# Optimization experiments

Measured on AMD Instinct MI355X. Metric: run time of the kernel, lower is better.

Reference implementation:

```python
import jax, jax.numpy as jnp
import numpy as np

IN_FEATURES = 4096
OUT_FEATURES = 11008
GROUP_SIZE = 32
M_TOKENS = 32
Q_MID = 8  # int4 midpoint: dequant = (q - 8) * scale + zero


def setup_inputs() -> dict:
    key = jax.random.key(0)
    k1, k2, k3, k4 = jax.random.split(key, 4)
    n_groups = IN_FEATURES // GROUP_SIZE
    inputs = {
        "input": jax.random.normal(k1, (M_TOKENS, IN_FEATURES), dtype=jnp.float32),
        "weight": jax.random.randint(k2, (OUT_FEATURES, IN_FEATURES), 0, 16, dtype=jnp.int32),
        "scales_and_zeros": jax.random.normal(k3, (n_groups, OUT_FEATURES, 2), dtype=jnp.float32),
        "bias": jax.random.normal(k4, (OUT_FEATURES,), dtype=jnp.float32),
        "group_size": GROUP_SIZE,
    }
    return inputs


def reference(input, weight, scales_and_zeros, bias, group_size):
    out_features, in_features = weight.shape
    n_groups = in_features // group_size
    # scales/zeros per (group, out) -> [out, n_groups]
    scale = scales_and_zeros[..., 0].T  # [out, G]
    zero = scales_and_zeros[..., 1].T   # [out, G]
    # dequantize int4 weight: w = (q - 8) * scale + zero, per group along in_features
    q = weight.astype(jnp.float32).reshape(out_features, n_groups, group_size)
    w_fp = (q - Q_MID) * scale[:, :, None] + zero[:, :, None]  # [out, G, gs]
    w_fp = w_fp.reshape(out_features, in_features)
    # y = x @ W^T + b
    y = jnp.einsum("bi,oi->bo", input, w_fp) + bias
    return y
```

## Files before the change

kernel.cpp:

```cpp
#include <hip/hip_runtime.h>
#include <hip/hip_bf16.h>
#include <stdint.h>

#define M_TOK 32
#define IN_F 4096
#define OUT_F 11008
#define NSPLIT 8
#define KRANGE (IN_F / NSPLIT)
#define NSTEP  (KRANGE / 32)
#define NKK    (IN_F / 32)

typedef __attribute__((ext_vector_type(8))) short bf16x8;
typedef __attribute__((ext_vector_type(4))) float f32x4;

__device__ inline uint32_t pack_bf16(float a, float b) {
    __hip_bfloat16 ha = __float2bfloat16(a);
    __hip_bfloat16 hb = __float2bfloat16(b);
    uint16_t ua = *(uint16_t*)&ha;
    uint16_t ub = *(uint16_t*)&hb;
    return (uint32_t)ua | ((uint32_t)ub << 16);
}

__global__ void init_out_kernel(const float* __restrict__ bias, float* __restrict__ out) {
    int o = blockIdx.x * 256 + threadIdx.x;
    int m = blockIdx.y;
    out[(size_t)m * OUT_F + o] = bias[o];
}

__global__ void prepack_a_kernel(const float* __restrict__ x, uint4* __restrict__ ws4) {
    int u  = blockIdx.x * 256 + threadIdx.x;
    int kk = u >> 6;
    int l  = u & 63;
    int lm = l & 15;
    int lq = l >> 4;
    int kb = kk * 32 + lq * 8;
    #pragma unroll
    for (int j = 0; j < 2; ++j) {
        const float* xp = x + (size_t)(lm + 16 * j) * IN_F + kb;
        union { uint4 q; uint32_t u[4]; } f;
        f.u[0] = pack_bf16(xp[0], xp[1]);
        f.u[1] = pack_bf16(xp[2], xp[3]);
        f.u[2] = pack_bf16(xp[4], xp[5]);
        f.u[3] = pack_bf16(xp[6], xp[7]);
        ws4[(size_t)kk * 128 + j * 64 + l] = f.q;
    }
}

__launch_bounds__(256)
__global__ void qgemm_kernel(const uint4* __restrict__ af,
                             const int* __restrict__ wq,
                             const float* __restrict__ sz,
                             float* __restrict__ out) {
    __shared__ int lds_w[2][64 * 32];

    const int bid = blockIdx.x;
    const int ks  = bid & (NSPLIT - 1);
    const int nb  = bid >> 3;
    const int t   = threadIdx.x;
    const int wv  = t >> 6;
    const int l   = t & 63;
    const int lm  = l & 15;
    const int lq  = l >> 4;

    const int row0 = nb * 64;
    const int row  = row0 + wv * 16 + lm;
    const int k0   = ks * KRANGE;

    const int rs    = t >> 3;
    const int cs    = t & 7;
    const int* gw0  = wq + (size_t)(row0 + rs) * IN_F + k0 + ((cs ^ (rs & 7)) * 4);
    const int* gw1  = gw0 + (size_t)32 * IN_F;

#define STAGE(buf, soff) do {                                                   \
    __builtin_amdgcn_global_load_lds(                                           \
        (const __attribute__((address_space(1))) int*)(gw0 + (soff)),           \
        (__attribute__((address_space(3))) int*)&lds_w[(buf)][wv * 256],        \
        16, 0, 0);                                                              \
    __builtin_amdgcn_global_load_lds(                                           \
        (const __attribute__((address_space(1))) int*)(gw1 + (soff)),           \
        (__attribute__((address_space(3))) int*)&lds_w[(buf)][1024 + wv * 256], \
        16, 0, 0);                                                              \
} while (0)

    const int rloc = wv * 16 + lm;
    const int c0   = rloc * 32 + (((2 * lq)     ^ (rloc & 7)) * 4);
    const int c1   = rloc * 32 + (((2 * lq + 1) ^ (rloc & 7)) * 4);

    const uint4* ap  = af + (size_t)(ks * NSTEP) * 128 + l;
    const float* szp = sz + ((size_t)(k0 >> 5) * OUT_F + row) * 2;

    f32x4 acc0 = {0.f, 0.f, 0.f, 0.f};
    f32x4 acc1 = {0.f, 0.f, 0.f, 0.f};

    STAGE(0, 0);
    int cur = 0;
    #pragma unroll 2
    for (int s = 0; s < NSTEP; ++s) {
        __syncthreads();
        if (s + 1 < NSTEP) STAGE(cur ^ 1, (s + 1) * 32);

        int4   q0 = *(const int4*)(&lds_w[cur][c0]);
        int4   q1 = *(const int4*)(&lds_w[cur][c1]);
        float2 sv = *(const float2*)(szp);
        union { uint4 q; bf16x8 v; } a0, a1;
        a0.q = ap[0];
        a1.q = ap[64];
        ap  += 128;
        szp += (size_t)OUT_F * 2;

        const float sc = sv.x;
        const float zp = sv.y - 8.0f * sv.x;

        union { bf16x8 v; uint32_t u[4]; } bf;
        bf.u[0] = pack_bf16((float)q0.x * sc + zp, (float)q0.y * sc + zp);
        bf.u[1] = pack_bf16((float)q0.z * sc + zp, (float)q0.w * sc + zp);
        bf.u[2] = pack_bf16((float)q1.x * sc + zp, (float)q1.y * sc + zp);
        bf.u[3] = pack_bf16((float)q1.z * sc + zp, (float)q1.w * sc + zp);

        acc0 = __builtin_amdgcn_mfma_f32_16x16x32_bf16(a0.v, bf.v, acc0, 0, 0, 0);
        acc1 = __builtin_amdgcn_mfma_f32_16x16x32_bf16(a1.v, bf.v, acc1, 0, 0, 0);
        cur ^= 1;
    }
#undef STAGE

    const int ocol = row;
    #pragma unroll
    for (int i = 0; i < 4; ++i) {
        int m0 = lq * 4 + i;
        atomicAdd(&out[(size_t)m0 * OUT_F + ocol], acc0[i]);
        atomicAdd(&out[(size_t)(16 + m0) * OUT_F + ocol], acc1[i]);
    }
}

extern "C" void kernel_launch(void* const* d_in, const int* in_sizes, int n_in,
                              void* d_out, int out_size, void* d_ws, size_t ws_size,
                              hipStream_t stream) {
    const float* x    = (const float*)d_in[0];
    const int*   wq   = (const int*)d_in[1];
    const float* sz   = (const float*)d_in[2];
    const float* bias = (const float*)d_in[3];
    float* out = (float*)d_out;
    uint4* af  = (uint4*)d_ws;

    prepack_a_kernel<<<dim3(NKK * 64 / 256), 256, 0, stream>>>(x, af);

    dim3 gi(OUT_F / 256, M_TOK);
    init_out_kernel<<<gi, 256, 0, stream>>>(bias, out);

    dim3 gg((OUT_F / 64) * NSPLIT);
    qgemm_kernel<<<gg, 256, 0, stream>>>((const uint4*)af, wq, sz, out);
}
```

Measured before the change: 275.0 us.

## Deepen weight LDS pipeline to four buffers with explicit vmcnt waits

Replaces the double-buffered weight staging with a four-buffer ring that keeps three tiles in flight, synchronised by hand-written s_waitcnt vmcnt and raw s_barrier plus sched_barrier. The goal is to hide more global-memory latency on the memory-bound int4 weight stream. The manual vmcnt counts assume that only the staging loads are outstanding. But the activation and scale loads inside each step are also vector memory ops, so the waits could be misaligned and unsafe. The change also quadruples LDS use per block.

```diff
diff --git a/kernel.cpp b/kernel.cpp
--- a/kernel.cpp
+++ b/kernel.cpp
@@ -9,6 +9,7 @@
 #define KRANGE (IN_F / NSPLIT)
 #define NSTEP  (KRANGE / 32)
 #define NKK    (IN_F / 32)
+#define NBUF   4
 
 typedef __attribute__((ext_vector_type(8))) short bf16x8;
 typedef __attribute__((ext_vector_type(4))) float f32x4;
@@ -51,7 +52,7 @@
                              const int* __restrict__ wq,
                              const float* __restrict__ sz,
                              float* __restrict__ out) {
-    __shared__ int lds_w[2][64 * 32];
+    __shared__ int lds_w[NBUF][64 * 32];
 
     const int bid = blockIdx.x;
     const int ks  = bid & (NSPLIT - 1);
@@ -71,15 +72,25 @@
     const int* gw0  = wq + (size_t)(row0 + rs) * IN_F + k0 + ((cs ^ (rs & 7)) * 4);
     const int* gw1  = gw0 + (size_t)32 * IN_F;
 
-#define STAGE(buf, soff) do {                                                   \
+#define STAGE(buf, tile) do {                                                   \
     __builtin_amdgcn_global_load_lds(                                           \
-        (const __attribute__((address_space(1))) int*)(gw0 + (soff)),           \
+        (const __attribute__((address_space(1))) int*)(gw0 + (tile) * 32),      \
         (__attribute__((address_space(3))) int*)&lds_w[(buf)][wv * 256],        \
         16, 0, 0);                                                              \
     __builtin_amdgcn_global_load_lds(                                           \
-        (const __attribute__((address_space(1))) int*)(gw1 + (soff)),           \
+        (const __attribute__((address_space(1))) int*)(gw1 + (tile) * 32),      \
         (__attribute__((address_space(3))) int*)&lds_w[(buf)][1024 + wv * 256], \
         16, 0, 0);                                                              \
+} while (0)
+
+#define WAITV(N) do {                                                           \
+    asm volatile("s_waitcnt vmcnt(" #N ")" ::: "memory");                       \
+    __builtin_amdgcn_sched_barrier(0);                                          \
+} while (0)
+
+#define BAR() do {                                                              \
+    __builtin_amdgcn_s_barrier();                                               \
+    __builtin_amdgcn_sched_barrier(0);                                          \
 } while (0)
 
     const int rloc = wv * 16 + lm;
@@ -92,36 +103,46 @@
     f32x4 acc0 = {0.f, 0.f, 0.f, 0.f};
     f32x4 acc1 = {0.f, 0.f, 0.f, 0.f};
 
+#define STEP_BODY(cb) do {                                                      \
+    int4   q0 = *(const int4*)(&lds_w[(cb)][c0]);                               \
+    int4   q1 = *(const int4*)(&lds_w[(cb)][c1]);                               \
+    float2 sv = *(const float2*)(szp);                                          \
+    union { uint4 q; bf16x8 v; } a0, a1;                                        \
+    a0.q = ap[0];                                                               \
+    a1.q = ap[64];                                                              \
+    ap  += 128;                                                                 \
+    szp += (size_t)OUT_F * 2;                                                   \
+    const float sc = sv.x;                                                      \
+    const float zp = sv.y - 8.0f * sv.x;                                        \
+    union { bf16x8 v; uint32_t u[4]; } bf;                                      \
+    bf.u[0] = pack_bf16((float)q0.x * sc + zp, (float)q0.y * sc + zp);          \
+    bf.u[1] = pack_bf16((float)q0.z * sc + zp, (float)q0.w * sc + zp);          \
+    bf.u[2] = pack_bf16((float)q1.x * sc + zp, (float)q1.y * sc + zp);          \
+    bf.u[3] = pack_bf16((float)q1.z * sc + zp, (float)q1.w * sc + zp);          \
+    acc0 = __builtin_amdgcn_mfma_f32_16x16x32_bf16(a0.v, bf.v, acc0, 0, 0, 0);  \
+    acc1 = __builtin_amdgcn_mfma_f32_16x16x32_bf16(a1.v, bf.v, acc1, 0, 0, 0);  \
+} while (0)
+
     STAGE(0, 0);
-    int cur = 0;
-    #pragma unroll 2
-    for (int s = 0; s < NSTEP; ++s) {
-        __syncthreads();
-        if (s + 1 < NSTEP) STAGE(cur ^ 1, (s + 1) * 32);
+    STAGE(1, 1);
+    STAGE(2, 2);
 
-        int4   q0 = *(const int4*)(&lds_w[cur][c0]);
-        int4   q1 = *(const int4*)(&lds_w[cur][c1]);
-        float2 sv = *(const float2*)(szp);
-        union { uint4 q; bf16x8 v; } a0, a1;
-        a0.q = ap[0];
-        a1.q = ap[64];
-        ap  += 128;
-        szp += (size_t)OUT_F * 2;
+    #pragma unroll 4
+    for (int s = 0; s < 12; ++s) {
+        WAITV(4);
+        BAR();
+        STAGE((s + 3) & 3, s + 3);
+        STEP_BODY(s & 3);
+    }
+    WAITV(4); BAR(); STAGE(3, 15); STEP_BODY(0);
+    WAITV(4); BAR(); STEP_BODY(1);
+    WAITV(2); BAR(); STEP_BODY(2);
+    WAITV(0); BAR(); STEP_BODY(3);
 
-        const float sc = sv.x;
-        const float zp = sv.y - 8.0f * sv.x;
-
-        union { bf16x8 v; uint32_t u[4]; } bf;
-        bf.u[0] = pack_bf16((float)q0.x * sc + zp, (float)q0.y * sc + zp);
-        bf.u[1] = pack_bf16((float)q0.z * sc + zp, (float)q0.w * sc + zp);
-        bf.u[2] = pack_bf16((float)q1.x * sc + zp, (float)q1.y * sc + zp);
-        bf.u[3] = pack_bf16((float)q1.z * sc + zp, (float)q1.w * sc + zp);
-
-        acc0 = __builtin_amdgcn_mfma_f32_16x16x32_bf16(a0.v, bf.v, acc0, 0, 0, 0);
-        acc1 = __builtin_amdgcn_mfma_f32_16x16x32_bf16(a1.v, bf.v, acc1, 0, 0, 0);
-        cur ^= 1;
-    }
+#undef STEP_BODY
 #undef STAGE
+#undef WAITV
+#undef BAR
 
     const int ocol = row;
     #pragma unroll
```

After: 272.7 us. No clear change (-0.8%).

## Repack int32 weights into nibble-packed layout before quantized GEMM

Applied to the files above, without the earlier changes.

Adds a per-call pre-pass that reads the int32 weight matrix and packs eight 4-bit values per 32-bit word into a layout matching the MFMA fragment order. The GEMM kernel then loads one packed word per lane per step directly from global memory, dropping the LDS double buffer and barriers, and unpacks with mask/shift. This aims to replace a latency-bound staged load of wide int32 data with a streaming repack plus a much lighter GEMM. It costs an extra kernel launch and workspace traffic for the packed weights.

```diff
diff --git a/kernel.cpp b/kernel.cpp
--- a/kernel.cpp
+++ b/kernel.cpp
@@ -46,13 +46,51 @@
     }
 }
 
+__global__ void repack_w_kernel(const int* __restrict__ wq, uint32_t* __restrict__ pw) {
+    __shared__ uint32_t lds32[32 * 16];
+    const int b     = blockIdx.x;
+    const int rg    = b >> 2;
+    const int chunk = b & 3;
+    const int t     = threadIdx.x;
+    const int row   = rg * 4 + (t >> 6);
+    const int K0    = chunk * 1024;
+    const int koff  = (t & 63) * 8;
+    const int s_l   = (t & 63) >> 2;
+    const int didx  = (t >> 6) * 4 + (t & 3);
+
+    #pragma unroll
+    for (int it = 0; it < 2; ++it) {
+        const int* ip = wq + (size_t)row * IN_F + K0 + it * 512 + koff;
+        int4 qa = *(const int4*)ip;
+        int4 qb = *(const int4*)(ip + 4);
+        uint32_t w = (uint32_t)(qa.x & 15)
+                   | ((uint32_t)(qa.y & 15) << 4)
+                   | ((uint32_t)(qa.z & 15) << 8)
+                   | ((uint32_t)(qa.w & 15) << 12)
+                   | ((uint32_t)(qb.x & 15) << 16)
+                   | ((uint32_t)(qb.y & 15) << 20)
+                   | ((uint32_t)(qb.z & 15) << 24)
+                   | ((uint32_t)(qb.w & 15) << 28);
+        lds32[(it * 16 + s_l) * 16 + didx] = w;
+    }
+    __syncthreads();
+
+    const int slice = t >> 3;
+    const int pair  = t & 7;
+    const int it_w  = slice >> 4;
+    const int s_w   = slice & 15;
+    const int ks_w  = chunk * 2 + it_w;
+    const int nb    = rg >> 4;
+    const int rloc0 = (rg & 15) * 4;
+    size_t base = ((size_t)(nb * 8 + ks_w) * 16 + s_w) * 256 + rloc0 * 4;
+    *(uint2*)(pw + base + pair * 2) = *(const uint2*)(&lds32[slice * 16 + pair * 2]);
+}
+
 __launch_bounds__(256)
 __global__ void qgemm_kernel(const uint4* __restrict__ af,
-                             const int* __restrict__ wq,
+                             const uint32_t* __restrict__ pw,
                              const float* __restrict__ sz,
                              float* __restrict__ out) {
-    __shared__ int lds_w[2][64 * 32];
-
     const int bid = blockIdx.x;
     const int ks  = bid & (NSPLIT - 1);
     const int nb  = bid >> 3;
@@ -61,67 +99,43 @@
     const int l   = t & 63;
     const int lm  = l & 15;
     const int lq  = l >> 4;
+    const int rloc = wv * 16 + lm;
+    const int row  = nb * 64 + rloc;
 
-    const int row0 = nb * 64;
-    const int row  = row0 + wv * 16 + lm;
-    const int k0   = ks * KRANGE;
-
-    const int rs    = t >> 3;
-    const int cs    = t & 7;
-    const int* gw0  = wq + (size_t)(row0 + rs) * IN_F + k0 + ((cs ^ (rs & 7)) * 4);
-    const int* gw1  = gw0 + (size_t)32 * IN_F;
-
-#define STAGE(buf, soff) do {                                                   \
-    __builtin_amdgcn_global_load_lds(                                           \
-        (const __attribute__((address_space(1))) int*)(gw0 + (soff)),           \
-        (__attribute__((address_space(3))) int*)&lds_w[(buf)][wv * 256],        \
-        16, 0, 0);                                                              \
-    __builtin_amdgcn_global_load_lds(                                           \
-        (const __attribute__((address_space(1))) int*)(gw1 + (soff)),           \
-        (__attribute__((address_space(3))) int*)&lds_w[(buf)][1024 + wv * 256], \
-        16, 0, 0);                                                              \
-} while (0)
-
-    const int rloc = wv * 16 + lm;
-    const int c0   = rloc * 32 + (((2 * lq)     ^ (rloc & 7)) * 4);
-    const int c1   = rloc * 32 + (((2 * lq + 1) ^ (rloc & 7)) * 4);
-
-    const uint4* ap  = af + (size_t)(ks * NSTEP) * 128 + l;
-    const float* szp = sz + ((size_t)(k0 >> 5) * OUT_F + row) * 2;
+    const uint32_t* wp = pw + ((size_t)(nb * 8 + ks) * 16) * 256 + rloc * 4 + lq;
+    const uint4*    ap = af + (size_t)ks * (NSTEP * 128) + l;
+    const float*   szp = sz + ((size_t)(ks * 16) * OUT_F + row) * 2;
 
     f32x4 acc0 = {0.f, 0.f, 0.f, 0.f};
     f32x4 acc1 = {0.f, 0.f, 0.f, 0.f};
 
-    STAGE(0, 0);
-    int cur = 0;
-    #pragma unroll 2
+    #pragma unroll 4
     for (int s = 0; s < NSTEP; ++s) {
-        __syncthreads();
-        if (s + 1 < NSTEP) STAGE(cur ^ 1, (s + 1) * 32);
-
-        int4   q0 = *(const int4*)(&lds_w[cur][c0]);
-        int4   q1 = *(const int4*)(&lds_w[cur][c1]);
-        float2 sv = *(const float2*)(szp);
+        uint32_t w  = wp[s * 256];
+        float2   sv = *(const float2*)(szp);
         union { uint4 q; bf16x8 v; } a0, a1;
-        a0.q = ap[0];
-        a1.q = ap[64];
-        ap  += 128;
+        a0.q = ap[s * 128];
+        a1.q = ap[s * 128 + 64];
         szp += (size_t)OUT_F * 2;
 
+        const uint32_t we = w & 0x0F0F0F0Fu;
+        const uint32_t no = (w >> 4) & 0x0F0F0F0Fu;
         const float sc = sv.x;
         const float zp = sv.y - 8.0f * sv.x;
 
         union { bf16x8 v; uint32_t u[4]; } bf;
-        bf.u[0] = pack_bf16((float)q0.x * sc + zp, (float)q0.y * sc + zp);
-        bf.u[1] = pack_bf16((float)q0.z * sc + zp, (float)q0.w * sc + zp);
-        bf.u[2] = pack_bf16((float)q1.x * sc + zp, (float)q1.y * sc + zp);
-        bf.u[3] = pack_bf16((float)q1.z * sc + zp, (float)q1.w * sc + zp);
+        bf.u[0] = pack_bf16((float)(we & 0xffu) * sc + zp,
+                            (float)(no & 0xffu) * sc + zp);
+        bf.u[1] = pack_bf16((float)((we >> 8) & 0xffu) * sc + zp,
+                            (float)((no >> 8) & 0xffu) * sc + zp);
+        bf.u[2] = pack_bf16((float)((we >> 16) & 0xffu) * sc + zp,
+                            (float)((no >> 16) & 0xffu) * sc + zp);
+        bf.u[3] = pack_bf16((float)(we >> 24) * sc + zp,
+                            (float)(no >> 24) * sc + zp);
 
         acc0 = __builtin_amdgcn_mfma_f32_16x16x32_bf16(a0.v, bf.v, acc0, 0, 0, 0);
         acc1 = __builtin_amdgcn_mfma_f32_16x16x32_bf16(a1.v, bf.v, acc1, 0, 0, 0);
-        cur ^= 1;
     }
-#undef STAGE
 
     const int ocol = row;
     #pragma unroll
@@ -140,13 +154,16 @@
     const float* sz   = (const float*)d_in[2];
     const float* bias = (const float*)d_in[3];
     float* out = (float*)d_out;
-    uint4* af  = (uint4*)d_ws;
+
+    uint4*    af = (uint4*)d_ws;
+    uint32_t* pw = (uint32_t*)((char*)d_ws + (1 << 20));
+
+    repack_w_kernel<<<dim3((OUT_F / 4) * 4), 256, 0, stream>>>(wq, pw);
 
     prepack_a_kernel<<<dim3(NKK * 64 / 256), 256, 0, stream>>>(x, af);
-
     dim3 gi(OUT_F / 256, M_TOK);
     init_out_kernel<<<gi, 256, 0, stream>>>(bias, out);
 
     dim3 gg((OUT_F / 64) * NSPLIT);
-    qgemm_kernel<<<gg, 256, 0, stream>>>((const uint4*)af, wq, sz, out);
+    qgemm_kernel<<<gg, 256, 0, stream>>>(af, pw, sz, out);
 }
```

New measurement: 295.0 us. 1.07x slower.
